# Kernel tuning notes

Measured on AMD Instinct MI355X. Metric: run time of the kernel, lower is better.

Reference implementation:

```python
import jax, jax.numpy as jnp
import numpy as np

N, L, S, H, D = 2, 2048, 2048, 8, 64

def elu_feature_map(x):
    return jax.nn.elu(x) + 1.0

def setup_inputs() -> dict:
    key = jax.random.key(0)
    k1, k2, k3, k4, k5 = jax.random.split(key, 5)
    return {
        "queries": jax.random.normal(k1, (N, L, H, D), dtype=jnp.float32),
        "keys": jax.random.normal(k2, (N, S, H, D), dtype=jnp.float32),
        "values": jax.random.normal(k3, (N, S, H, D), dtype=jnp.float32),
        "q_mask": jnp.ones((N, L), dtype=jnp.float32),
        "kv_mask": jnp.ones((N, S), dtype=jnp.float32),
        "W": jax.random.normal(k4, (1, 2), dtype=jnp.float32) * 0.5,  # nn.Linear(2,1) weight
        "b": jax.random.normal(k5, (1,), dtype=jnp.float32) * 0.5,    # nn.Linear(2,1) bias
    }

def reference(queries, keys, values, q_mask, kv_mask, W, b):
    # feature map: elu(x) + 1
    Q = elu_feature_map(queries) * q_mask[:, :, None, None]   # [N,L,H,D]
    K = elu_feature_map(keys) * kv_mask[:, :, None, None]     # [N,S,H,D]
    queries_m = queries * q_mask[:, :, None, None]
    values_m = values * kv_mask[:, :, None, None]  # masked but unused downstream (as in original)
    del values_m
    # full QK score tensor [N,L,S,H]
    qk = jnp.einsum('nlhd,nshd->nlsh', Q, K)
    qk_mean = jnp.mean(qk, axis=2)  # [N,L,H]
    qk_max = jnp.max(qk, axis=2)    # [N,L,H]
    stats = jnp.stack([qk_mean, qk_max], axis=-1)  # [N,L,H,2]
    gate = jax.nn.sigmoid(jnp.einsum('nlhe,oe->nlho', stats, W) + b)  # [N,L,H,1]
    atten = gate[..., 0]  # [N,L,H]
    return queries_m * atten[..., None]  # [N,L,H,D]
```

## Files before the change

### kernel.cpp

```cpp
#include <hip/hip_runtime.h>
#include <math.h>

#define N_ 2
#define L_ 2048
#define S_ 2048
#define H_ 8
#define D_ 64

#define BLK_L 256
#define BS 64
#define SSPLIT 4

typedef __attribute__((ext_vector_type(8))) short short8;
typedef __attribute__((ext_vector_type(4))) float floatx4;

__device__ __forceinline__ float feat(float x) {
    return x > 0.0f ? x + 1.0f : __expf(x);
}
__device__ __forceinline__ short f2bf(float x) {
    unsigned u = __float_as_uint(x);
    unsigned r = (u + 0x7fffu + ((u >> 16) & 1u)) >> 16;
    return (short)r;
}
__device__ __forceinline__ float bf2f(short h) {
    return __uint_as_float(((unsigned)(unsigned short)h) << 16);
}
__device__ __forceinline__ void gload_lds16(const void* g, void* l) {
    __builtin_amdgcn_global_load_lds(
        (__attribute__((address_space(1))) void*)g,
        (__attribute__((address_space(3))) void*)l, 16, 0, 0);
}

__global__ __launch_bounds__(256) void featk_kernel(
        const float* __restrict__ K, const float* __restrict__ kvmask,
        short* __restrict__ Khi, short* __restrict__ Klo,
        float* __restrict__ Ksum) {
    __shared__ float sm[64][68];
    int nh = blockIdx.x;
    int z  = blockIdx.y;
    int n = nh >> 3, h = nh & 7;
    int t = threadIdx.x;
    int srow = t >> 2, g = t & 3;
    int s = z * 64 + srow;

    float km = kvmask[n * S_ + s];
    const float* kp = K + (((size_t)n * S_ + s) * H_ + h) * D_ + g * 16;
    float fv[16];
    #pragma unroll
    for (int j = 0; j < 4; ++j) {
        float4 v = *(const float4*)(kp + j * 4);
        fv[4 * j + 0] = feat(v.x) * km;
        fv[4 * j + 1] = feat(v.y) * km;
        fv[4 * j + 2] = feat(v.z) * km;
        fv[4 * j + 3] = feat(v.w) * km;
    }
    short8 h0, h1, l0, l1;
    #pragma unroll
    for (int j = 0; j < 8; ++j) {
        short hb = f2bf(fv[j]);
        h0[j] = hb;  l0[j] = f2bf(fv[j] - bf2f(hb));
        short hb2 = f2bf(fv[8 + j]);
        h1[j] = hb2; l1[j] = f2bf(fv[8 + j] - bf2f(hb2));
    }
    size_t rowbase = ((size_t)nh * S_ + s) * (size_t)D_;
    int rx = srow & 7;
    *(short8*)(Khi + rowbase + ((((2 * g)    ) ^ rx) << 3)) = h0;
    *(short8*)(Khi + rowbase + ((((2 * g) + 1) ^ rx) << 3)) = h1;
    *(short8*)(Klo + rowbase + ((((2 * g)    ) ^ rx) << 3)) = l0;
    *(short8*)(Klo + rowbase + ((((2 * g) + 1) ^ rx) << 3)) = l1;

    #pragma unroll
    for (int j2 = 0; j2 < 4; ++j2)
        *(float4*)&sm[srow][g * 16 + 4 * j2] =
            make_float4(fv[4 * j2], fv[4 * j2 + 1], fv[4 * j2 + 2], fv[4 * j2 + 3]);
    __syncthreads();
    if (t < 64) {
        float tot = 0.f;
        #pragma unroll
        for (int r = 0; r < 64; ++r) tot += sm[r][t];
        atomicAdd(&Ksum[nh * 64 + t], tot);
    }
}

__global__ __launch_bounds__(256) void rowmax_mfma(
        const float* __restrict__ Q, const short* __restrict__ Khi,
        const short* __restrict__ Klo, const float* __restrict__ qmask,
        float* __restrict__ rowmaxg) {
    __shared__ __align__(16) char lds[2][16384];

    int flat = blockIdx.x + (blockIdx.y << 3) + (blockIdx.z << 7);
    int nid  = ((flat & 7) << 6) | (flat >> 3);
    int bx = nid & 7;
    int nh = (nid >> 3) & 15;
    int z  = nid >> 7;

    int n = nh >> 3, h = nh & 7;
    int t = threadIdx.x;
    int w = t >> 6, lane = t & 63;
    int quad = lane >> 4, l16 = lane & 15;
    int lblock = bx * BLK_L;

    const char* gKh = (const char*)Khi + ((size_t)nh * S_ + (size_t)z * (S_ / SSPLIT)) * 128;
    const char* gKl = (const char*)Klo + ((size_t)nh * S_ + (size_t)z * (S_ / SSPLIT)) * 128;
    int sidx = w << 2;

    auto stage = [&](int tile, int db) {
        #pragma unroll
        for (int c = 0; c < 4; ++c) {
            int idx = sidx | c;
            const char* src = (idx < 8 ? gKh : gKl)
                              + tile * 8192 + ((idx & 7) << 10) + (lane << 4);
            gload_lds16(src, &lds[db][idx << 10]);
        }
    };

    stage(0, 0);

    short8 Ah[4][2], Al[4][2];
    #pragma unroll
    for (int lsub = 0; lsub < 4; ++lsub) {
        int lrow = lblock + w * 64 + lsub * 16 + l16;
        float qm = qmask[n * L_ + lrow];
        const float* qp = Q + (((size_t)n * L_ + lrow) * H_ + h) * D_ + quad * 8;
        #pragma unroll
        for (int ks = 0; ks < 2; ++ks) {
            float4 v0 = *(const float4*)(qp + ks * 32);
            float4 v1 = *(const float4*)(qp + ks * 32 + 4);
            float fv[8];
            fv[0] = feat(v0.x) * qm; fv[1] = feat(v0.y) * qm;
            fv[2] = feat(v0.z) * qm; fv[3] = feat(v0.w) * qm;
            fv[4] = feat(v1.x) * qm; fv[5] = feat(v1.y) * qm;
            fv[6] = feat(v1.z) * qm; fv[7] = feat(v1.w) * qm;
            short8 hi, lo;
            #pragma unroll
            for (int j = 0; j < 8; ++j) {
                short hb = f2bf(fv[j]);
                hi[j] = hb;
                lo[j] = f2bf(fv[j] - bf2f(hb));
            }
            Ah[lsub][ks] = hi;
            Al[lsub][ks] = lo;
        }
    }

    int boff[4][2];
    #pragma unroll
    for (int ssub = 0; ssub < 4; ++ssub) {
        int row = ssub * 16 + l16;
        int rx = l16 & 7;
        boff[ssub][0] = row * 128 + ((quad ^ rx) << 4);
        boff[ssub][1] = row * 128 + (((quad + 4) ^ rx) << 4);
    }

    float rmax[4][4];
    #pragma unroll
    for (int i = 0; i < 4; ++i)
        #pragma unroll
        for (int r = 0; r < 4; ++r) rmax[i][r] = 0.f;

    __syncthreads();

    const int tiles = S_ / SSPLIT / BS;
    for (int tile = 0; tile < tiles; ++tile) {
        int db = tile & 1;
        if (tile + 1 < tiles) stage(tile + 1, db ^ 1);
        const char* hp = lds[db];
        const char* lp = lds[db] + 8192;
        #pragma unroll
        for (int ssub = 0; ssub < 4; ++ssub) {
            short8 Bh0 = *(const short8*)(hp + boff[ssub][0]);
            short8 Bh1 = *(const short8*)(hp + boff[ssub][1]);
            short8 Bl0 = *(const short8*)(lp + boff[ssub][0]);
            short8 Bl1 = *(const short8*)(lp + boff[ssub][1]);
            #pragma unroll
            for (int lsub = 0; lsub < 4; ++lsub) {
                floatx4 acc = {0.f, 0.f, 0.f, 0.f};
                acc = __builtin_amdgcn_mfma_f32_16x16x32_bf16(Ah[lsub][0], Bh0, acc, 0, 0, 0);
                acc = __builtin_amdgcn_mfma_f32_16x16x32_bf16(Ah[lsub][1], Bh1, acc, 0, 0, 0);
                acc = __builtin_amdgcn_mfma_f32_16x16x32_bf16(Ah[lsub][0], Bl0, acc, 0, 0, 0);
                acc = __builtin_amdgcn_mfma_f32_16x16x32_bf16(Ah[lsub][1], Bl1, acc, 0, 0, 0);
                acc = __builtin_amdgcn_mfma_f32_16x16x32_bf16(Al[lsub][0], Bh0, acc, 0, 0, 0);
                acc = __builtin_amdgcn_mfma_f32_16x16x32_bf16(Al[lsub][1], Bh1, acc, 0, 0, 0);
                #pragma unroll
                for (int r = 0; r < 4; ++r)
                    rmax[lsub][r] = fmaxf(rmax[lsub][r], acc[r]);
            }
        }
        __syncthreads();
    }

    #pragma unroll
    for (int lsub = 0; lsub < 4; ++lsub)
        #pragma unroll
        for (int r = 0; r < 4; ++r) {
            float m = rmax[lsub][r];
            m = fmaxf(m, __shfl_xor(m, 1, 64));
            m = fmaxf(m, __shfl_xor(m, 2, 64));
            m = fmaxf(m, __shfl_xor(m, 4, 64));
            m = fmaxf(m, __shfl_xor(m, 8, 64));
            if (l16 == 0) {
                int l = lblock + w * 64 + lsub * 16 + quad * 4 + r;
                atomicMax((unsigned*)&rowmaxg[(size_t)nh * L_ + l],
                          __float_as_uint(m));
            }
        }
}

__global__ __launch_bounds__(256) void finalize_kernel(
        const float* __restrict__ Q, const float* __restrict__ qmask,
        const float* __restrict__ Ksum, const float* __restrict__ rowmaxg,
        const float* __restrict__ W, const float* __restrict__ b,
        float* __restrict__ out) {
    int t = threadIdx.x;
    int lane = t & 63;
    int wid = (blockIdx.x << 2) | (t >> 6);
    int n = wid / (L_ * H_);
    int lh = wid % (L_ * H_);
    int l = lh / H_, h = lh % H_;

    float q = Q[(size_t)wid * 64 + lane];
    float qm = qmask[n * L_ + l];
    float p = feat(q) * qm * Ksum[(n * H_ + h) * 64 + lane];
    #pragma unroll
    for (int off = 32; off > 0; off >>= 1)
        p += __shfl_xor(p, off, 64);
    float mean = p * (1.0f / S_);
    float mx = rowmaxg[((size_t)n * H_ + h) * L_ + l];
    float zz = W[0] * mean + W[1] * mx + b[0];
    float g = 1.0f / (1.0f + __expf(-zz));
    out[(size_t)wid * 64 + lane] = q * qm * g;
}

extern "C" void kernel_launch(void* const* d_in, const int* in_sizes, int n_in,
                              void* d_out, int out_size, void* d_ws, size_t ws_size,
                              hipStream_t stream) {
    const float* Q      = (const float*)d_in[0];
    const float* K      = (const float*)d_in[1];
    const float* qmask  = (const float*)d_in[3];
    const float* kvmask = (const float*)d_in[4];
    const float* W      = (const float*)d_in[5];
    const float* b      = (const float*)d_in[6];
    float* out = (float*)d_out;

    float* Ksum   = (float*)d_ws;
    float* rowmax = (float*)d_ws + 1024;
    short* Khi    = (short*)((float*)d_ws + 1024 + 32768);
    short* Klo    = Khi + (size_t)N_ * H_ * S_ * D_;

    hipMemsetAsync(d_ws, 0, (1024 + (size_t)N_ * H_ * L_) * sizeof(float), stream);

    featk_kernel<<<dim3(N_ * H_, S_ / 64), 256, 0, stream>>>(K, kvmask, Khi, Klo, Ksum);
    rowmax_mfma<<<dim3(L_ / BLK_L, N_ * H_, SSPLIT), 256, 0, stream>>>(
        Q, Khi, Klo, qmask, rowmax);
    finalize_kernel<<<dim3(N_ * L_ * H_ / 4), 256, 0, stream>>>(
        Q, qmask, Ksum, rowmax, W, b, out);
}
```

Measured before the change: 115.4 us.

## Switch rowmax split-precision MFMA from bf16 16x16x32 to fp16 32x32x16 tiles

The QK rowmax kernel now splits features into fp16 hi/lo parts instead of bf16 and uses 32x32x16 fp16 MFMA with 16-element accumulators, replacing the 16x16x32 bf16 tiling. The LDS fragment offsets and the cross-lane max reduction are recomputed for the new output layout. Larger tiles reuse each loaded operand more and cut LDS reads per FLOP, but raise register pressure, so launch bounds now request 2 blocks per SM. The featk column reduction is also split across all 256 threads instead of 64. fp16 has a narrower exponent range than bf16, which is acceptable here because the elu+1 features are positive and moderate in size.

```diff
diff --git a/kernel.cpp b/kernel.cpp
--- a/kernel.cpp
+++ b/kernel.cpp
@@ -12,18 +12,11 @@
 #define SSPLIT 4
 
 typedef __attribute__((ext_vector_type(8))) short short8;
-typedef __attribute__((ext_vector_type(4))) float floatx4;
+typedef _Float16 half8 __attribute__((ext_vector_type(8)));
+typedef __attribute__((ext_vector_type(16))) float floatx16;
 
 __device__ __forceinline__ float feat(float x) {
     return x > 0.0f ? x + 1.0f : __expf(x);
-}
-__device__ __forceinline__ short f2bf(float x) {
-    unsigned u = __float_as_uint(x);
-    unsigned r = (u + 0x7fffu + ((u >> 16) & 1u)) >> 16;
-    return (short)r;
-}
-__device__ __forceinline__ float bf2f(short h) {
-    return __uint_as_float(((unsigned)(unsigned short)h) << 16);
 }
 __device__ __forceinline__ void gload_lds16(const void* g, void* l) {
     __builtin_amdgcn_global_load_lds(
@@ -36,6 +29,7 @@
         short* __restrict__ Khi, short* __restrict__ Klo,
         float* __restrict__ Ksum) {
     __shared__ float sm[64][68];
+    __shared__ float sm2[256];
     int nh = blockIdx.x;
     int z  = blockIdx.y;
     int n = nh >> 3, h = nh & 7;
@@ -54,35 +48,41 @@
         fv[4 * j + 2] = feat(v.z) * km;
         fv[4 * j + 3] = feat(v.w) * km;
     }
-    short8 h0, h1, l0, l1;
+    half8 h0, h1, l0, l1;
     #pragma unroll
     for (int j = 0; j < 8; ++j) {
-        short hb = f2bf(fv[j]);
-        h0[j] = hb;  l0[j] = f2bf(fv[j] - bf2f(hb));
-        short hb2 = f2bf(fv[8 + j]);
-        h1[j] = hb2; l1[j] = f2bf(fv[8 + j] - bf2f(hb2));
+        _Float16 hb = (_Float16)fv[j];
+        h0[j] = hb;  l0[j] = (_Float16)(fv[j] - (float)hb);
+        _Float16 hb2 = (_Float16)fv[8 + j];
+        h1[j] = hb2; l1[j] = (_Float16)(fv[8 + j] - (float)hb2);
     }
     size_t rowbase = ((size_t)nh * S_ + s) * (size_t)D_;
     int rx = srow & 7;
-    *(short8*)(Khi + rowbase + ((((2 * g)    ) ^ rx) << 3)) = h0;
-    *(short8*)(Khi + rowbase + ((((2 * g) + 1) ^ rx) << 3)) = h1;
-    *(short8*)(Klo + rowbase + ((((2 * g)    ) ^ rx) << 3)) = l0;
-    *(short8*)(Klo + rowbase + ((((2 * g) + 1) ^ rx) << 3)) = l1;
+    *(half8*)(Khi + rowbase + ((((2 * g)    ) ^ rx) << 3)) = h0;
+    *(half8*)(Khi + rowbase + ((((2 * g) + 1) ^ rx) << 3)) = h1;
+    *(half8*)(Klo + rowbase + ((((2 * g)    ) ^ rx) << 3)) = l0;
+    *(half8*)(Klo + rowbase + ((((2 * g) + 1) ^ rx) << 3)) = l1;
 
     #pragma unroll
     for (int j2 = 0; j2 < 4; ++j2)
         *(float4*)&sm[srow][g * 16 + 4 * j2] =
             make_float4(fv[4 * j2], fv[4 * j2 + 1], fv[4 * j2 + 2], fv[4 * j2 + 3]);
     __syncthreads();
+    {
+        int d = t & 63, grp = t >> 6;
+        float part = 0.f;
+        #pragma unroll
+        for (int k = 0; k < 16; ++k) part += sm[grp * 16 + k][d];
+        sm2[t] = part;
+    }
+    __syncthreads();
     if (t < 64) {
-        float tot = 0.f;
-        #pragma unroll
-        for (int r = 0; r < 64; ++r) tot += sm[r][t];
+        float tot = sm2[t] + sm2[t + 64] + sm2[t + 128] + sm2[t + 192];
         atomicAdd(&Ksum[nh * 64 + t], tot);
     }
 }
 
-__global__ __launch_bounds__(256) void rowmax_mfma(
+__global__ __launch_bounds__(256, 2) void rowmax_mfma(
         const float* __restrict__ Q, const short* __restrict__ Khi,
         const short* __restrict__ Klo, const float* __restrict__ qmask,
         float* __restrict__ rowmaxg) {
@@ -97,7 +97,7 @@
     int n = nh >> 3, h = nh & 7;
     int t = threadIdx.x;
     int w = t >> 6, lane = t & 63;
-    int quad = lane >> 4, l16 = lane & 15;
+    int c31 = lane & 31, hi32 = lane >> 5;
     int lblock = bx * BLK_L;
 
     const char* gKh = (const char*)Khi + ((size_t)nh * S_ + (size_t)z * (S_ / SSPLIT)) * 128;
@@ -116,47 +116,49 @@
 
     stage(0, 0);
 
-    short8 Ah[4][2], Al[4][2];
-    #pragma unroll
-    for (int lsub = 0; lsub < 4; ++lsub) {
-        int lrow = lblock + w * 64 + lsub * 16 + l16;
+    half8 Ah[2][4], Al[2][4];
+    #pragma unroll
+    for (int lt = 0; lt < 2; ++lt) {
+        int lrow = lblock + w * 64 + lt * 32 + c31;
         float qm = qmask[n * L_ + lrow];
-        const float* qp = Q + (((size_t)n * L_ + lrow) * H_ + h) * D_ + quad * 8;
-        #pragma unroll
-        for (int ks = 0; ks < 2; ++ks) {
-            float4 v0 = *(const float4*)(qp + ks * 32);
-            float4 v1 = *(const float4*)(qp + ks * 32 + 4);
+        const float* qp = Q + (((size_t)n * L_ + lrow) * H_ + h) * D_ + hi32 * 8;
+        #pragma unroll
+        for (int ks = 0; ks < 4; ++ks) {
+            float4 v0 = *(const float4*)(qp + ks * 16);
+            float4 v1 = *(const float4*)(qp + ks * 16 + 4);
             float fv[8];
             fv[0] = feat(v0.x) * qm; fv[1] = feat(v0.y) * qm;
             fv[2] = feat(v0.z) * qm; fv[3] = feat(v0.w) * qm;
             fv[4] = feat(v1.x) * qm; fv[5] = feat(v1.y) * qm;
             fv[6] = feat(v1.z) * qm; fv[7] = feat(v1.w) * qm;
-            short8 hi, lo;
+            half8 hi, lo;
             #pragma unroll
             for (int j = 0; j < 8; ++j) {
-                short hb = f2bf(fv[j]);
+                _Float16 hb = (_Float16)fv[j];
                 hi[j] = hb;
-                lo[j] = f2bf(fv[j] - bf2f(hb));
-            }
-            Ah[lsub][ks] = hi;
-            Al[lsub][ks] = lo;
-        }
-    }
-
-    int boff[4][2];
-    #pragma unroll
-    for (int ssub = 0; ssub < 4; ++ssub) {
-        int row = ssub * 16 + l16;
-        int rx = l16 & 7;
-        boff[ssub][0] = row * 128 + ((quad ^ rx) << 4);
-        boff[ssub][1] = row * 128 + (((quad + 4) ^ rx) << 4);
-    }
-
-    float rmax[4][4];
-    #pragma unroll
-    for (int i = 0; i < 4; ++i)
-        #pragma unroll
-        for (int r = 0; r < 4; ++r) rmax[i][r] = 0.f;
+                lo[j] = (_Float16)(fv[j] - (float)hb);
+            }
+            Ah[lt][ks] = hi;
+            Al[lt][ks] = lo;
+        }
+    }
+
+    int boff[2][4];
+    #pragma unroll
+    for (int st = 0; st < 2; ++st)
+        #pragma unroll
+        for (int ks = 0; ks < 4; ++ks) {
+            int row = st * 32 + c31;
+            boff[st][ks] = row * 128 + (((2 * ks + hi32) ^ (row & 7)) << 4);
+        }
+
+    float rmax[2][16];
+    #pragma unroll
+    for (int i = 0; i < 2; ++i)
+        #pragma unroll
+        for (int r = 0; r < 16; ++r) rmax[i][r] = 0.f;
+
+    const floatx16 Z = {0.f};
 
     __syncthreads();
 
@@ -167,39 +169,48 @@
         const char* hp = lds[db];
         const char* lp = lds[db] + 8192;
         #pragma unroll
-        for (int ssub = 0; ssub < 4; ++ssub) {
-            short8 Bh0 = *(const short8*)(hp + boff[ssub][0]);
-            short8 Bh1 = *(const short8*)(hp + boff[ssub][1]);
-            short8 Bl0 = *(const short8*)(lp + boff[ssub][0]);
-            short8 Bl1 = *(const short8*)(lp + boff[ssub][1]);
+        for (int st = 0; st < 2; ++st) {
+            half8 Bh[4], Bl[4];
             #pragma unroll
-            for (int lsub = 0; lsub < 4; ++lsub) {
-                floatx4 acc = {0.f, 0.f, 0.f, 0.f};
-                acc = __builtin_amdgcn_mfma_f32_16x16x32_bf16(Ah[lsub][0], Bh0, acc, 0, 0, 0);
-                acc = __builtin_amdgcn_mfma_f32_16x16x32_bf16(Ah[lsub][1], Bh1, acc, 0, 0, 0);
-                acc = __builtin_amdgcn_mfma_f32_16x16x32_bf16(Ah[lsub][0], Bl0, acc, 0, 0, 0);
-                acc = __builtin_amdgcn_mfma_f32_16x16x32_bf16(Ah[lsub][1], Bl1, acc, 0, 0, 0);
-                acc = __builtin_amdgcn_mfma_f32_16x16x32_bf16(Al[lsub][0], Bh0, acc, 0, 0, 0);
-                acc = __builtin_amdgcn_mfma_f32_16x16x32_bf16(Al[lsub][1], Bh1, acc, 0, 0, 0);
+            for (int ks = 0; ks < 4; ++ks) {
+                Bh[ks] = *(const half8*)(hp + boff[st][ks]);
+                Bl[ks] = *(const half8*)(lp + boff[st][ks]);
+            }
+            #pragma unroll
+            for (int lt = 0; lt < 2; ++lt) {
+                floatx16 acc;
+                acc = __builtin_amdgcn_mfma_f32_32x32x16_f16(Ah[lt][0], Bh[0], Z,   0, 0, 0);
+                acc = __builtin_amdgcn_mfma_f32_32x32x16_f16(Ah[lt][1], Bh[1], acc, 0, 0, 0);
+                acc = __builtin_amdgcn_mfma_f32_32x32x16_f16(Ah[lt][2], Bh[2], acc, 0, 0, 0);
+                acc = __builtin_amdgcn_mfma_f32_32x32x16_f16(Ah[lt][3], Bh[3], acc, 0, 0, 0);
+                acc = __builtin_amdgcn_mfma_f32_32x32x16_f16(Ah[lt][0], Bl[0], acc, 0, 0, 0);
+                acc = __builtin_amdgcn_mfma_f32_32x32x16_f16(Ah[lt][1], Bl[1], acc, 0, 0, 0);
+                acc = __builtin_amdgcn_mfma_f32_32x32x16_f16(Ah[lt][2], Bl[2], acc, 0, 0, 0);
+                acc = __builtin_amdgcn_mfma_f32_32x32x16_f16(Ah[lt][3], Bl[3], acc, 0, 0, 0);
+                acc = __builtin_amdgcn_mfma_f32_32x32x16_f16(Al[lt][0], Bh[0], acc, 0, 0, 0);
+                acc = __builtin_amdgcn_mfma_f32_32x32x16_f16(Al[lt][1], Bh[1], acc, 0, 0, 0);
+                acc = __builtin_amdgcn_mfma_f32_32x32x16_f16(Al[lt][2], Bh[2], acc, 0, 0, 0);
+                acc = __builtin_amdgcn_mfma_f32_32x32x16_f16(Al[lt][3], Bh[3], acc, 0, 0, 0);
                 #pragma unroll
-                for (int r = 0; r < 4; ++r)
-                    rmax[lsub][r] = fmaxf(rmax[lsub][r], acc[r]);
+                for (int r = 0; r < 16; ++r)
+                    rmax[lt][r] = fmaxf(rmax[lt][r], acc[r]);
             }
         }
         __syncthreads();
     }
 
     #pragma unroll
-    for (int lsub = 0; lsub < 4; ++lsub)
-        #pragma unroll
-        for (int r = 0; r < 4; ++r) {
-            float m = rmax[lsub][r];
+    for (int lt = 0; lt < 2; ++lt)
+        #pragma unroll
+        for (int r = 0; r < 16; ++r) {
+            float m = rmax[lt][r];
             m = fmaxf(m, __shfl_xor(m, 1, 64));
             m = fmaxf(m, __shfl_xor(m, 2, 64));
             m = fmaxf(m, __shfl_xor(m, 4, 64));
             m = fmaxf(m, __shfl_xor(m, 8, 64));
-            if (l16 == 0) {
-                int l = lblock + w * 64 + lsub * 16 + quad * 4 + r;
+            m = fmaxf(m, __shfl_xor(m, 16, 64));
+            if (c31 == 0) {
+                int l = lblock + w * 64 + lt * 32 + (r & 3) + ((r >> 2) << 3) + (hi32 << 2);
                 atomicMax((unsigned*)&rowmaxg[(size_t)nh * L_ + l],
                           __float_as_uint(m));
             }
```

Result: slower. 118.5 us (+2.7%).

## Replace atomics and memset with partial buffers; vectorize finalize kernel

Applied to the files above, without the earlier changes.

Removes the workspace memset by having featk write per-block partial K sums and rowmax write per-split partial maxima instead of using atomicAdd/atomicMax. One rowmax block per head reduces the K partials into Ksum, and finalize reduces the four rowmax partials directly. The finalize kernel is also changed to have each thread handle a float4, with a 16-lane shuffle reduction. Small reductions move into other kernels in exchange for dropping a memset launch and atomic traffic.

```diff
diff --git a/kernel.cpp b/kernel.cpp
--- a/kernel.cpp
+++ b/kernel.cpp
@@ -34,8 +34,9 @@
 __global__ __launch_bounds__(256) void featk_kernel(
         const float* __restrict__ K, const float* __restrict__ kvmask,
         short* __restrict__ Khi, short* __restrict__ Klo,
-        float* __restrict__ Ksum) {
+        float* __restrict__ Kpart) {
     __shared__ float sm[64][68];
+    __shared__ float sm2[256];
     int nh = blockIdx.x;
     int z  = blockIdx.y;
     int n = nh >> 3, h = nh & 7;
@@ -74,18 +75,25 @@
         *(float4*)&sm[srow][g * 16 + 4 * j2] =
             make_float4(fv[4 * j2], fv[4 * j2 + 1], fv[4 * j2 + 2], fv[4 * j2 + 3]);
     __syncthreads();
+    {
+        int d = t & 63, grp = t >> 6;
+        float part = 0.f;
+        #pragma unroll
+        for (int k = 0; k < 16; ++k) part += sm[grp * 16 + k][d];
+        sm2[t] = part;
+    }
+    __syncthreads();
     if (t < 64) {
-        float tot = 0.f;
-        #pragma unroll
-        for (int r = 0; r < 64; ++r) tot += sm[r][t];
-        atomicAdd(&Ksum[nh * 64 + t], tot);
+        float tot = sm2[t] + sm2[t + 64] + sm2[t + 128] + sm2[t + 192];
+        Kpart[(nh * 32 + z) * 64 + t] = tot;
     }
 }
 
 __global__ __launch_bounds__(256) void rowmax_mfma(
         const float* __restrict__ Q, const short* __restrict__ Khi,
         const short* __restrict__ Klo, const float* __restrict__ qmask,
-        float* __restrict__ rowmaxg) {
+        const float* __restrict__ Kpart, float* __restrict__ Ksum,
+        float* __restrict__ rmax_part) {
     __shared__ __align__(16) char lds[2][16384];
 
     int flat = blockIdx.x + (blockIdx.y << 3) + (blockIdx.z << 7);
@@ -115,6 +123,14 @@
     };
 
     stage(0, 0);
+
+    if (bx == 0 && z == 0 && t < 64) {
+        float s = 0.f;
+        #pragma unroll
+        for (int zz = 0; zz < 32; ++zz)
+            s += Kpart[(nh * 32 + zz) * 64 + t];
+        Ksum[nh * 64 + t] = s;
+    }
 
     short8 Ah[4][2], Al[4][2];
     #pragma unroll
@@ -200,35 +216,47 @@
             m = fmaxf(m, __shfl_xor(m, 8, 64));
             if (l16 == 0) {
                 int l = lblock + w * 64 + lsub * 16 + quad * 4 + r;
-                atomicMax((unsigned*)&rowmaxg[(size_t)nh * L_ + l],
-                          __float_as_uint(m));
+                rmax_part[((size_t)(z * 16 + nh)) * L_ + l] = m;
             }
         }
 }
 
 __global__ __launch_bounds__(256) void finalize_kernel(
         const float* __restrict__ Q, const float* __restrict__ qmask,
-        const float* __restrict__ Ksum, const float* __restrict__ rowmaxg,
+        const float* __restrict__ Ksum, const float* __restrict__ rmax_part,
         const float* __restrict__ W, const float* __restrict__ b,
         float* __restrict__ out) {
     int t = threadIdx.x;
-    int lane = t & 63;
-    int wid = (blockIdx.x << 2) | (t >> 6);
+    int fid = blockIdx.x * 256 + t;
+    int wid = fid >> 4;
+    int sub = fid & 15;
     int n = wid / (L_ * H_);
     int lh = wid % (L_ * H_);
     int l = lh / H_, h = lh % H_;
-
-    float q = Q[(size_t)wid * 64 + lane];
+    int nh = n * H_ + h;
+
+    float4 q4 = ((const float4*)Q)[fid];
     float qm = qmask[n * L_ + l];
-    float p = feat(q) * qm * Ksum[(n * H_ + h) * 64 + lane];
-    #pragma unroll
-    for (int off = 32; off > 0; off >>= 1)
-        p += __shfl_xor(p, off, 64);
+    float4 ks4 = ((const float4*)(Ksum + nh * 64))[sub];
+    float p = feat(q4.x) * ks4.x + feat(q4.y) * ks4.y
+            + feat(q4.z) * ks4.z + feat(q4.w) * ks4.w;
+    p *= qm;
+    p += __shfl_xor(p, 1, 64);
+    p += __shfl_xor(p, 2, 64);
+    p += __shfl_xor(p, 4, 64);
+    p += __shfl_xor(p, 8, 64);
     float mean = p * (1.0f / S_);
-    float mx = rowmaxg[((size_t)n * H_ + h) * L_ + l];
+    float mx = fmaxf(
+        fmaxf(rmax_part[((size_t)(0 * 16 + nh)) * L_ + l],
+              rmax_part[((size_t)(1 * 16 + nh)) * L_ + l]),
+        fmaxf(rmax_part[((size_t)(2 * 16 + nh)) * L_ + l],
+              rmax_part[((size_t)(3 * 16 + nh)) * L_ + l]));
     float zz = W[0] * mean + W[1] * mx + b[0];
     float g = 1.0f / (1.0f + __expf(-zz));
-    out[(size_t)wid * 64 + lane] = q * qm * g;
+    float4 o;
+    o.x = q4.x * qm * g; o.y = q4.y * qm * g;
+    o.z = q4.z * qm * g; o.w = q4.w * qm * g;
+    ((float4*)out)[fid] = o;
 }
 
 extern "C" void kernel_launch(void* const* d_in, const int* in_sizes, int n_in,
@@ -242,16 +270,15 @@
     const float* b      = (const float*)d_in[6];
     float* out = (float*)d_out;
 
-    float* Ksum   = (float*)d_ws;
-    float* rowmax = (float*)d_ws + 1024;
-    short* Khi    = (short*)((float*)d_ws + 1024 + 32768);
-    short* Klo    = Khi + (size_t)N_ * H_ * S_ * D_;
-
-    hipMemsetAsync(d_ws, 0, (1024 + (size_t)N_ * H_ * L_) * sizeof(float), stream);
-
-    featk_kernel<<<dim3(N_ * H_, S_ / 64), 256, 0, stream>>>(K, kvmask, Khi, Klo, Ksum);
+    float* Ksum      = (float*)d_ws;
+    float* Kpart     = Ksum + 1024;
+    float* rmax_part = Kpart + 32768;
+    short* Khi       = (short*)(rmax_part + 131072);
+    short* Klo       = Khi + (size_t)N_ * H_ * S_ * D_;
+
+    featk_kernel<<<dim3(N_ * H_, S_ / 64), 256, 0, stream>>>(K, kvmask, Khi, Klo, Kpart);
     rowmax_mfma<<<dim3(L_ / BLK_L, N_ * H_, SSPLIT), 256, 0, stream>>>(
-        Q, Khi, Klo, qmask, rowmax);
-    finalize_kernel<<<dim3(N_ * L_ * H_ / 4), 256, 0, stream>>>(
-        Q, qmask, Ksum, rowmax, W, b, out);
-}
+        Q, Khi, Klo, qmask, Kpart, Ksum, rmax_part);
+    finalize_kernel<<<dim3((N_ * L_ * H_ * D_ / 4) / 256), 256, 0, stream>>>(
+        Q, qmask, Ksum, rmax_part, W, b, out);
+}
```

New measurement: 111.1 us, median of 2. -3.7%, faster.
